# Optimization experiments

Measured on AMD Instinct MI355X. Metric: run time of the kernel, lower is better.

The kernel has to match this reference:

```python
import jax, jax.numpy as jnp
import numpy as np

D_MODEL, D_QKV, N_HEADS, D_FFN = 2048, 128, 16, 8192
B, L = 2, 2048
EPS = 1e-8
ROPE_THETA = 10000.0


def _rope_cos_sin(seq_len, dim, dtype):
    # interleaved RoPE (rotary_embedding_torch default): pairs (0,1),(2,3),...
    inv_freq = ROPE_THETA ** (-jnp.arange(0, dim, 2, dtype=jnp.float32) / dim)
    ang = jnp.arange(seq_len, dtype=jnp.float32)[:, None] * inv_freq[None, :]  # [L, dim/2]
    return jnp.cos(ang).astype(dtype), jnp.sin(ang).astype(dtype)


def _apply_rope(t, cos, sin):
    # t: [b, h, l, d]; cos/sin: [l, d/2]
    t1, t2 = t[..., 0::2], t[..., 1::2]
    r1 = t1 * cos - t2 * sin
    r2 = t1 * sin + t2 * cos
    return jnp.stack([r1, r2], axis=-1).reshape(t.shape)


def setup_inputs() -> dict:
    key = jax.random.key(0)
    ks = jax.random.split(key, 5)
    d_out = D_QKV * N_HEADS * 3 + D_FFN * 2  # 22528
    return {
        "x": jax.random.normal(ks[0], (B, L, D_MODEL), dtype=jnp.float32),
        "g": jnp.ones((D_MODEL,), dtype=jnp.float32),
        "W_dense": jax.random.normal(ks[1], (d_out, D_MODEL), dtype=jnp.float32) * 0.02,
        "b_dense": jnp.zeros((d_out,), dtype=jnp.float32),
        "W_attn_out": jax.random.normal(ks[2], (D_MODEL, D_QKV * N_HEADS), dtype=jnp.float32) * 0.02,
        "W_ffn_out": jax.random.normal(ks[3], (D_MODEL, D_FFN), dtype=jnp.float32) * 0.02,
    }


def reference(x, g, W_dense, b_dense, W_attn_out, W_ffn_out):
    # RMSNorm (torch.norm variant): x / clamp(||x|| * d^-0.5, eps) * g
    norm = jnp.sqrt(jnp.sum(x * x, axis=-1, keepdims=True)) * (D_MODEL ** -0.5)
    normed = x / jnp.maximum(norm, EPS) * g

    h = jnp.einsum('bld,od->blo', normed, W_dense) + b_dense  # [B, L, 22528]
    dh = D_QKV * N_HEADS
    q, k, v, a, b_gate = jnp.split(h, [dh, 2 * dh, 3 * dh, 3 * dh + D_FFN], axis=-1)

    def to_heads(t):
        return t.reshape(B, L, N_HEADS, D_QKV).transpose(0, 2, 1, 3)  # [b,h,l,d]

    q, k, v = to_heads(q), to_heads(k), to_heads(v)
    cos, sin = _rope_cos_sin(L, D_QKV, x.dtype)
    q = _apply_rope(q, cos, sin)
    k = _apply_rope(k, cos, sin)

    scale = 1.0 / jnp.sqrt(jnp.asarray(D_QKV, dtype=x.dtype))
    scores = jnp.einsum('bhqd,bhkd->bhqk', q, k) * scale
    causal = jnp.tril(jnp.ones((L, L), dtype=bool))
    scores = jnp.where(causal, scores, jnp.asarray(-jnp.inf, dtype=scores.dtype))
    probs = jax.nn.softmax(scores, axis=-1)
    attn = jnp.einsum('bhqk,bhkd->bqhd', probs, v).reshape(B, L, dh)

    attn_out = jnp.einsum('blk,ok->blo', attn, W_attn_out)
    ffn_out = jnp.einsum('blf,of->blo', a * jax.nn.silu(b_gate), W_ffn_out)
    return x + attn_out + ffn_out
```

## Files before the change

kernel.cpp:

```cpp
#include <hip/hip_runtime.h>
#include <hip/hip_bf16.h>
#include <cmath>

typedef __bf16 bf16;
typedef __attribute__((ext_vector_type(8))) __bf16 bf16x8;
typedef __attribute__((ext_vector_type(4))) float f32x4;
typedef unsigned int u32;
typedef unsigned short u16;

#define D_MODEL 2048
#define NH 16
#define DQ 128
#define DH 2048
#define DFFN 8192
#define DOUT 22528
#define BATCH 2
#define SEQ 2048
#define NROWS 4096

__device__ __forceinline__ void gload16(const void* g, void* l) {
    __builtin_amdgcn_global_load_lds((__attribute__((address_space(1))) const void*)g,
                                     (__attribute__((address_space(3))) void*)l, 16, 0, 0);
}

__device__ __forceinline__ float bf2f(u16 u) {
    union { u32 i; float f; } c; c.i = ((u32)u) << 16; return c.f;
}

__global__ __launch_bounds__(256) void cvt_f32_bf16(const float* __restrict__ in,
                                                    bf16* __restrict__ out) {
    size_t i = ((size_t)blockIdx.x * 256 + threadIdx.x) * 8;
    float4 a = *(const float4*)(in + i);
    float4 b = *(const float4*)(in + i + 4);
    bf16x8 o;
    o[0]=(bf16)a.x; o[1]=(bf16)a.y; o[2]=(bf16)a.z; o[3]=(bf16)a.w;
    o[4]=(bf16)b.x; o[5]=(bf16)b.y; o[6]=(bf16)b.z; o[7]=(bf16)b.w;
    *(bf16x8*)(out + i) = o;
}

__global__ __launch_bounds__(256) void rmsnorm_k(const float* __restrict__ x,
                                                 const float* __restrict__ g,
                                                 bf16* __restrict__ out) {
    __shared__ float red[4];
    const int row = blockIdx.x;
    const int t = threadIdx.x;
    const float* xr = x + (size_t)row * D_MODEL;
    float4 v0 = *(const float4*)(xr + t*8);
    float4 v1 = *(const float4*)(xr + t*8 + 4);
    float ss = v0.x*v0.x + v0.y*v0.y + v0.z*v0.z + v0.w*v0.w
             + v1.x*v1.x + v1.y*v1.y + v1.z*v1.z + v1.w*v1.w;
    #pragma unroll
    for (int m = 32; m >= 1; m >>= 1) ss += __shfl_xor(ss, m);
    if ((t & 63) == 0) red[t >> 6] = ss;
    __syncthreads();
    float tot = red[0] + red[1] + red[2] + red[3];
    float norm = sqrtf(tot) * 0.022097086912079608f;
    float inv = 1.0f / fmaxf(norm, 1e-8f);
    float4 g0 = *(const float4*)(g + t*8);
    float4 g1 = *(const float4*)(g + t*8 + 4);
    bf16x8 o;
    o[0]=(bf16)(v0.x*inv*g0.x); o[1]=(bf16)(v0.y*inv*g0.y);
    o[2]=(bf16)(v0.z*inv*g0.z); o[3]=(bf16)(v0.w*inv*g0.w);
    o[4]=(bf16)(v1.x*inv*g1.x); o[5]=(bf16)(v1.y*inv*g1.y);
    o[6]=(bf16)(v1.z*inv*g1.z); o[7]=(bf16)(v1.w*inv*g1.w);
    *(bf16x8*)(out + (size_t)row * D_MODEL + t*8) = o;
}

#define VMW(n)  asm volatile("s_waitcnt vmcnt(" #n ")" ::: "memory")
#define LGK0()  asm volatile("s_waitcnt lgkmcnt(0)" ::: "memory")
#define BARX()  { asm volatile("" ::: "memory"); __builtin_amdgcn_s_barrier(); asm volatile("" ::: "memory"); }

#define SLINE_A(c_, t_) \
    gload16(Asrc + (size_t)((c_)*64)*K + (size_t)(t_)*64, \
            smem + (((t_)&1)<<16) + (c_)*8192 + wid*1024);
#define SLINE_B(c_, t_) \
    gload16(Bsrc + (size_t)((c_)*64)*K + (size_t)(t_)*64, \
            smem + (((t_)&1)<<16) + 32768 + (c_)*8192 + wid*1024);

#define PH_READS_B() \
    _Pragma("unroll") for (int n = 0; n < 4; ++n) { \
        const char* p_ = bb + (wn*64 + n*16 + la) * 128; \
        bfr[n][0] = *(const bf16x8*)(p_ + pg0); \
        bfr[n][1] = *(const bf16x8*)(p_ + pg1); }

#define PH_READS_A(qd_) \
    _Pragma("unroll") for (int mm = 0; mm < 2; ++mm) { \
        const char* p_ = ab + (wm*128 + ((qd_)*2 + mm)*16 + la) * 128; \
        af[mm][0] = *(const bf16x8*)(p_ + pg0); \
        af[mm][1] = *(const bf16x8*)(p_ + pg1); }

#define PH_MFMA(qd_) \
    __builtin_amdgcn_s_setprio(1); \
    _Pragma("unroll") for (int mm = 0; mm < 2; ++mm) \
        _Pragma("unroll") for (int n = 0; n < 4; ++n) { \
            acc[(qd_)*2+mm][n] = __builtin_amdgcn_mfma_f32_16x16x32_bf16(af[mm][0], bfr[n][0], acc[(qd_)*2+mm][n], 0, 0, 0); \
            acc[(qd_)*2+mm][n] = __builtin_amdgcn_mfma_f32_16x16x32_bf16(af[mm][1], bfr[n][1], acc[(qd_)*2+mm][n], 0, 0, 0); } \
    __builtin_amdgcn_s_setprio(0);

template<int MODE>
__global__ __launch_bounds__(512, 2) void gemm256f(
    const bf16* __restrict__ A, const bf16* __restrict__ B,
    int M, int N, int K, int nbx,
    const float* __restrict__ bias, bf16* __restrict__ outb,
    const float* __restrict__ addsrc, float* __restrict__ outf)
{
    __shared__ char smem[131072];
    const int tid = threadIdx.x;
    const int wid = tid >> 6, lane = tid & 63;
    const int la = lane & 15, hi = lane >> 4;
    const int wm = wid >> 2, wn = wid & 3;

    const int nwg = gridDim.x;
    const int cpx = nwg >> 3;
    const int bI = blockIdx.x;
    const int wg = (bI & 7) * cpx + (bI >> 3);
    const int bm = wg / nbx, bn = wg % nbx;
    const size_t m0 = (size_t)bm * 256, n0 = (size_t)bn * 256;

    const int lr = lane >> 3, lg = lane & 7;
    const int sg = lg ^ lr;
    const bf16* Asrc = A + (m0 + wid*8 + lr) * (size_t)K + sg*8;
    const bf16* Bsrc = B + (n0 + wid*8 + lr) * (size_t)K + sg*8;

    const int pg0 = (hi ^ (la & 7)) << 4;
    const int pg1 = ((4 + hi) ^ (la & 7)) << 4;

    f32x4 acc[8][4] = {};
    const int NT = K >> 6;

    SLINE_A(0,0); SLINE_A(2,0);
    SLINE_B(0,0); SLINE_B(1,0);
    SLINE_B(2,0); SLINE_B(3,0);
    SLINE_A(1,0); SLINE_A(3,0);
    VMW(2);
    BARX();

    bf16x8 bfr[4][2];
    bf16x8 af[2][2];

    #pragma unroll 1
    for (int t = 0; t < NT - 1; ++t) {
        const char* ab = smem + ((t & 1) << 16);
        const char* bb = ab + 32768;
        const int nx = t + 1;
        PH_READS_B(); PH_READS_A(0);
        SLINE_A(0,nx); SLINE_A(2,nx);
        BARX(); LGK0(); PH_MFMA(0); BARX();
        PH_READS_A(1);
        SLINE_B(0,nx); SLINE_B(1,nx);
        BARX(); LGK0(); PH_MFMA(1); VMW(4); BARX();
        PH_READS_A(2);
        SLINE_B(2,nx); SLINE_B(3,nx);
        BARX(); LGK0(); PH_MFMA(2); BARX();
        PH_READS_A(3);
        SLINE_A(1,nx); SLINE_A(3,nx);
        BARX(); LGK0(); PH_MFMA(3); VMW(2); BARX();
    }
    {
        const int t = NT - 1;
        const char* ab = smem + ((t & 1) << 16);
        const char* bb = ab + 32768;
        PH_READS_B(); PH_READS_A(0);
        BARX(); LGK0(); PH_MFMA(0); BARX();
        PH_READS_A(1);
        BARX(); LGK0(); PH_MFMA(1); VMW(0); BARX();
        PH_READS_A(2);
        BARX(); LGK0(); PH_MFMA(2); BARX();
        PH_READS_A(3);
        BARX(); LGK0(); PH_MFMA(3); BARX();
    }

    #pragma unroll
    for (int mf = 0; mf < 8; ++mf) {
        const size_t row = m0 + wm*128 + mf*16 + hi*4;
        #pragma unroll
        for (int nf = 0; nf < 4; ++nf) {
            const size_t col = n0 + wn*64 + nf*16 + la;
            if (MODE == 0) {
                const float bv = bias[col];
                #pragma unroll
                for (int r = 0; r < 4; ++r)
                    outb[(row + r) * N + col] = (bf16)(acc[mf][nf][r] + bv);
            } else {
                #pragma unroll
                for (int r = 0; r < 4; ++r) {
                    const size_t off = (row + r) * N + col;
                    outf[off] = addsrc[off] + acc[mf][nf][r];
                }
            }
        }
    }
}

template<int MODE>
__global__ __launch_bounds__(256) void gemm_bt(
    const bf16* __restrict__ A, const bf16* __restrict__ B,
    int M, int N, int K,
    const float* __restrict__ bias, bf16* __restrict__ outb,
    const float* __restrict__ addsrc, float* __restrict__ outf)
{
    __shared__ bf16 As[128][32];
    __shared__ bf16 Bs[128][32];
    const int tid = threadIdx.x;
    const int wid = tid >> 6, lane = tid & 63;
    const int la = lane & 15, hi = lane >> 4;
    const int m0 = blockIdx.y * 128, n0 = blockIdx.x * 128;
    const int wr = (wid >> 1) * 64, wc = (wid & 1) * 64;
    f32x4 acc[4][4] = {};
    const int idx0 = tid, idx1 = 256 + tid;
    const int r0 = idx0 >> 2, c0 = (idx0 & 3) << 3;
    const int r1 = idx1 >> 2, c1 = (idx1 & 3) << 3;
    const bf16* Ap0 = A + (size_t)(m0 + r0) * K + c0;
    const bf16* Ap1 = A + (size_t)(m0 + r1) * K + c1;
    const bf16* Bp0 = B + (size_t)(n0 + r0) * K + c0;
    const bf16* Bp1 = B + (size_t)(n0 + r1) * K + c1;
    char* asb = (char*)As + wid * 1024;
    char* bsb = (char*)Bs + wid * 1024;

    for (int k0 = 0; k0 < K; k0 += 32) {
        __syncthreads();
        gload16(Ap0 + k0, asb);
        gload16(Ap1 + k0, asb + 4096);
        gload16(Bp0 + k0, bsb);
        gload16(Bp1 + k0, bsb + 4096);
        __syncthreads();
        bf16x8 af[4], bfr[4];
        #pragma unroll
        for (int m = 0; m < 4; ++m) af[m] = *(const bf16x8*)&As[wr + m*16 + la][hi*8];
        #pragma unroll
        for (int n = 0; n < 4; ++n) bfr[n] = *(const bf16x8*)&Bs[wc + n*16 + la][hi*8];
        #pragma unroll
        for (int m = 0; m < 4; ++m)
            #pragma unroll
            for (int n = 0; n < 4; ++n)
                acc[m][n] = __builtin_amdgcn_mfma_f32_16x16x32_bf16(af[m], bfr[n], acc[m][n], 0, 0, 0);
    }

    #pragma unroll
    for (int m = 0; m < 4; ++m) {
        const int row = m0 + wr + m*16 + hi*4;
        #pragma unroll
        for (int n = 0; n < 4; ++n) {
            const int col = n0 + wc + n*16 + la;
            if (MODE == 0) {
                const float bv = bias[col];
                #pragma unroll
                for (int r = 0; r < 4; ++r)
                    outb[(size_t)(row + r) * N + col] = (bf16)(acc[m][n][r] + bv);
            } else {
                #pragma unroll
                for (int r = 0; r < 4; ++r) {
                    const size_t off = (size_t)(row + r) * N + col;
                    outf[off] = addsrc[off] + acc[m][n][r];
                }
            }
        }
    }
}

__global__ __launch_bounds__(256) void rope_table(float* __restrict__ ctab,
                                                  float* __restrict__ stab) {
    int idx = blockIdx.x * 256 + threadIdx.x;
    int l = idx >> 6, i = idx & 63;
    float inv = powf(10000.0f, -(float)i / 64.0f);
    float ang = (float)l * inv;
    float s, c;
    sincosf(ang, &s, &c);
    ctab[idx] = c; stab[idx] = s;
}

__device__ __forceinline__ u32 rope_pair(u32 u, float c, float s) {
    float t1 = bf2f((u16)(u & 0xffff));
    float t2 = bf2f((u16)(u >> 16));
    float r1 = t1 * c - t2 * s;
    float r2 = t1 * s + t2 * c;
    bf16 b1 = (bf16)r1, b2 = (bf16)r2;
    return (u32)__builtin_bit_cast(u16, b1) | ((u32)__builtin_bit_cast(u16, b2) << 16);
}

__global__ __launch_bounds__(256) void rope_qk(const bf16* __restrict__ h,
                                               const float* __restrict__ ctab,
                                               const float* __restrict__ stab,
                                               bf16* __restrict__ qb, bf16* __restrict__ kb) {
    int idx = blockIdx.x * 256 + threadIdx.x;
    int i  = idx & 63;
    int hh = (idx >> 6) & 15;
    int l  = (idx >> 10) & 2047;
    int b  = idx >> 21;
    size_t hrow = (size_t)(b * SEQ + l) * DOUT;
    float c = ctab[l*64 + i], s = stab[l*64 + i];
    u32 uq = *(const u32*)(h + hrow + hh*DQ + 2*i);
    u32 uk = *(const u32*)(h + hrow + DH + hh*DQ + 2*i);
    size_t orow = ((size_t)(b*NH + hh) * SEQ + l) * DQ + 2*i;
    *(u32*)(qb + orow) = rope_pair(uq, c, s);
    *(u32*)(kb + orow) = rope_pair(uk, c, s);
}

__global__ __launch_bounds__(256) void v_transpose(const bf16* __restrict__ h,
                                                   bf16* __restrict__ vt) {
    __shared__ u32 lds[64][68];
    const int lt = blockIdx.x, bh = blockIdx.y;
    const int b = bh >> 4, hh = bh & 15;
    const int t = threadIdx.x;
    const bf16* src = h + (size_t)(b * SEQ + lt * 64) * DOUT + 2*DH + hh * DQ;
    #pragma unroll
    for (int i = 0; i < 4; ++i) {
        int j = i*256 + t;
        int l = j >> 4, ch = j & 15;
        uint4 v = *(const uint4*)(src + (size_t)l * DOUT + ch*8);
        *(uint4*)&lds[l][ch*4] = v;
    }
    __syncthreads();
    bf16* dst = vt + (size_t)bh * DQ * SEQ + lt * 64;
    #pragma unroll
    for (int i = 0; i < 4; ++i) {
        int j = i*256 + t;
        int d = j >> 3, lc = j & 7;
        u32 out[4];
        #pragma unroll
        for (int m = 0; m < 4; ++m) {
            u32 a0 = lds[lc*8 + 2*m][d >> 1];
            u32 a1 = lds[lc*8 + 2*m + 1][d >> 1];
            u16 s0 = (d & 1) ? (u16)(a0 >> 16) : (u16)(a0 & 0xffff);
            u16 s1 = (d & 1) ? (u16)(a1 >> 16) : (u16)(a1 & 0xffff);
            out[m] = (u32)s0 | ((u32)s1 << 16);
        }
        *(uint4*)(dst + (size_t)d * SEQ + lc*8) = *(uint4*)out;
    }
}

__global__ __launch_bounds__(256) void silu_k(const bf16* __restrict__ h,
                                              bf16* __restrict__ ag) {
    size_t idx = ((size_t)blockIdx.x * 256 + threadIdx.x) * 8;
    int r = (int)(idx >> 13);
    int f = (int)(idx & 8191);
    const bf16* hr = h + (size_t)r * DOUT + 3*DH;
    bf16x8 va = *(const bf16x8*)(hr + f);
    bf16x8 vb = *(const bf16x8*)(hr + DFFN + f);
    bf16x8 o;
    #pragma unroll
    for (int j = 0; j < 8; ++j) {
        float a = (float)va[j];
        float b = (float)vb[j];
        float sil = b / (1.0f + __expf(-b));
        o[j] = (bf16)(a * sil);
    }
    *(bf16x8*)(ag + idx) = o;
}

__global__ __launch_bounds__(256) void attn_fa(const bf16* __restrict__ Q,
                                               const bf16* __restrict__ Kb,
                                               const bf16* __restrict__ Vt,
                                               bf16* __restrict__ O) {
    __shared__ bf16 Ks[64][128];
    __shared__ bf16 Vts[128][64];
    __shared__ bf16 Ps[4][16][64];
    const int qt = blockIdx.x, bh = blockIdx.y;
    const int b = bh >> 4, hh = bh & 15;
    const int tid = threadIdx.x, wid = tid >> 6, lane = tid & 63;
    const int la = lane & 15, hi = lane >> 4;
    const bf16* Qp = Q + (size_t)bh * SEQ * DQ;
    const bf16* Kp = Kb + (size_t)bh * SEQ * DQ;
    const bf16* Vp = Vt + (size_t)bh * DQ * SEQ;
    const int q0w = qt * 64 + wid * 16;

    bf16x8 qf[4];
    #pragma unroll
    for (int s = 0; s < 4; ++s)
        qf[s] = *(const bf16x8*)(Qp + (size_t)(q0w + la) * DQ + s*32 + hi*8);

    f32x4 acc_o[8] = {};
    float m_run[4] = {-1e30f, -1e30f, -1e30f, -1e30f};
    float l_run[4] = {0.f, 0.f, 0.f, 0.f};
    const float scale = 0.08838834764831845f;

    const int nk = qt + 1;
    for (int kt = 0; kt < nk; ++kt) {
        const int k0 = kt * 64;
        __syncthreads();
        #pragma unroll
        for (int i = 0; i < 4; ++i) {
            int j = i*256 + tid;
            int kr = j >> 4, jg = j & 15;
            gload16(Kp + (size_t)(k0 + kr) * DQ + ((jg ^ (kr & 7)) << 3),
                    (char*)Ks + i*4096 + wid*1024);
            int d = j >> 3, vg = j & 7;
            gload16(Vp + (size_t)d * SEQ + k0 + ((vg ^ (d & 7)) << 3),
                    (char*)Vts + i*4096 + wid*1024);
        }
        __syncthreads();

        f32x4 sacc[4] = {};
        __builtin_amdgcn_s_setprio(1);
        #pragma unroll
        for (int g = 0; g < 4; ++g) {
            const int krow = g*16 + la;
            #pragma unroll
            for (int s = 0; s < 4; ++s) {
                bf16x8 kf = *(const bf16x8*)((const char*)Ks + krow*256 + (((s*4 + hi) ^ (la & 7)) << 4));
                sacc[g] = __builtin_amdgcn_mfma_f32_16x16x32_bf16(qf[s], kf, sacc[g], 0, 0, 0);
            }
        }
        __builtin_amdgcn_s_setprio(0);

        float mnew[4];
        #pragma unroll
        for (int r = 0; r < 4; ++r) mnew[r] = m_run[r];
        #pragma unroll
        for (int g = 0; g < 4; ++g)
            #pragma unroll
            for (int r = 0; r < 4; ++r) {
                float sv = sacc[g][r] * scale;
                int qi = q0w + hi*4 + r;
                int ki = k0 + g*16 + la;
                sv = (ki <= qi) ? sv : -1e30f;
                sacc[g][r] = sv;
                mnew[r] = fmaxf(mnew[r], sv);
            }
        #pragma unroll
        for (int r = 0; r < 4; ++r) {
            float v = mnew[r];
            v = fmaxf(v, __shfl_xor(v, 1));
            v = fmaxf(v, __shfl_xor(v, 2));
            v = fmaxf(v, __shfl_xor(v, 4));
            v = fmaxf(v, __shfl_xor(v, 8));
            mnew[r] = v;
        }
        float resc[4], lsum[4];
        #pragma unroll
        for (int r = 0; r < 4; ++r) {
            resc[r] = __expf(m_run[r] - mnew[r]);
            m_run[r] = mnew[r];
            lsum[r] = 0.f;
        }
        #pragma unroll
        for (int g = 0; g < 4; ++g)
            #pragma unroll
            for (int r = 0; r < 4; ++r) {
                float p = __expf(sacc[g][r] - mnew[r]);
                sacc[g][r] = p;
                lsum[r] += p;
            }
        #pragma unroll
        for (int r = 0; r < 4; ++r) {
            float v = lsum[r];
            v += __shfl_xor(v, 1); v += __shfl_xor(v, 2);
            v += __shfl_xor(v, 4); v += __shfl_xor(v, 8);
            l_run[r] = l_run[r] * resc[r] + v;
        }
        #pragma unroll
        for (int g = 0; g < 4; ++g)
            #pragma unroll
            for (int r = 0; r < 4; ++r) {
                int prow = hi*4 + r;
                int pcol = (g*16 + la) ^ ((prow & 7) << 3);
                Ps[wid][prow][pcol] = (bf16)sacc[g][r];
            }
        #pragma unroll
        for (int n = 0; n < 8; ++n)
            #pragma unroll
            for (int r = 0; r < 4; ++r) acc_o[n][r] *= resc[r];
        __builtin_amdgcn_s_setprio(1);
        #pragma unroll
        for (int kk = 0; kk < 2; ++kk) {
            bf16x8 pf = *(const bf16x8*)((const char*)&Ps[wid][0][0] + la*128 +
                                         (((kk*32 + hi*8) ^ ((la & 7) << 3)) << 1));
            #pragma unroll
            for (int n = 0; n < 8; ++n) {
                const int vrow = n*16 + la;
                bf16x8 vf = *(const bf16x8*)((const char*)Vts + vrow*128 + (((kk*4 + hi) ^ (la & 7)) << 4));
                acc_o[n] = __builtin_amdgcn_mfma_f32_16x16x32_bf16(pf, vf, acc_o[n], 0, 0, 0);
            }
        }
        __builtin_amdgcn_s_setprio(0);
    }

    bf16* Op = O + (size_t)b * SEQ * DH + (size_t)hh * DQ;
    #pragma unroll
    for (int r = 0; r < 4; ++r) {
        int qi = q0w + hi*4 + r;
        float invl = 1.0f / l_run[r];
        #pragma unroll
        for (int n = 0; n < 8; ++n)
            Op[(size_t)qi * DH + n*16 + la] = (bf16)(acc_o[n][r] * invl);
    }
}

extern "C" void kernel_launch(void* const* d_in, const int* in_sizes, int n_in,
                              void* d_out, int out_size, void* d_ws, size_t ws_size,
                              hipStream_t stream) {
    const float* x       = (const float*)d_in[0];
    const float* g       = (const float*)d_in[1];
    const float* W_dense = (const float*)d_in[2];
    const float* b_dense = (const float*)d_in[3];
    const float* W_attn  = (const float*)d_in[4];
    const float* W_ffn   = (const float*)d_in[5];
    float* out = (float*)d_out;

    char* ws = (char*)d_ws;
    bf16* normed  = (bf16*)(ws + 0);
    bf16* Wd_b    = (bf16*)(ws + 16777216);
    bf16* Wa_b    = (bf16*)(ws + 109051904);
    bf16* Wf_b    = (bf16*)(ws + 117440512);
    bf16* h_b     = (bf16*)(ws + 150994944);
    bf16* ag_b    = (bf16*)(ws + 335544320);
    float* ctab   = (float*)(ws + 402653184);
    float* stab   = (float*)(ws + 403177472);
    bf16* q_b  = (bf16*)(ws + 16777216);
    bf16* k_b  = (bf16*)(ws + 16777216 + 16777216);
    bf16* vt_b = (bf16*)(ws + 16777216 + 33554432);
    bf16* attn_b = normed;

    cvt_f32_bf16<<<46137344/2048, 256, 0, stream>>>(W_dense, Wd_b);
    cvt_f32_bf16<<<4194304/2048, 256, 0, stream>>>(W_attn, Wa_b);
    cvt_f32_bf16<<<16777216/2048, 256, 0, stream>>>(W_ffn, Wf_b);
    rmsnorm_k<<<NROWS, 256, 0, stream>>>(x, g, normed);
    {
        dim3 grid((NROWS/256) * (DOUT/256));
        gemm256f<0><<<grid, 512, 0, stream>>>(normed, Wd_b, NROWS, DOUT, D_MODEL,
                                              DOUT/256, b_dense, h_b, nullptr, nullptr);
    }
    rope_table<<<SEQ*64/256, 256, 0, stream>>>(ctab, stab);
    rope_qk<<<4194304/256, 256, 0, stream>>>(h_b, ctab, stab, q_b, k_b);
    {
        dim3 grid(SEQ/64, BATCH*NH);
        v_transpose<<<grid, 256, 0, stream>>>(h_b, vt_b);
    }
    silu_k<<<(size_t)NROWS*DFFN/8/256, 256, 0, stream>>>(h_b, ag_b);
    {
        dim3 grid(SEQ/64, BATCH*NH);
        attn_fa<<<grid, 256, 0, stream>>>(q_b, k_b, vt_b, attn_b);
    }
    {
        dim3 grid(D_MODEL/128, NROWS/128);
        gemm_bt<1><<<grid, 256, 0, stream>>>(attn_b, Wa_b, NROWS, D_MODEL, DH,
                                             nullptr, nullptr, x, out);
    }
    {
        dim3 grid(D_MODEL/128, NROWS/128);
        gemm_bt<1><<<grid, 256, 0, stream>>>(ag_b, Wf_b, NROWS, D_MODEL, DFFN,
                                             nullptr, nullptr, out, out);
    }
}
```

Before: 952.8 us.

## Fuse attention and FFN output projections into one pipelined GEMM

```diff
diff --git a/kernel.cpp b/kernel.cpp
--- a/kernel.cpp
+++ b/kernel.cpp
@@ -26,6 +26,10 @@
 __device__ __forceinline__ float bf2f(u16 u) {
     union { u32 i; float f; } c; c.i = ((u32)u) << 16; return c.f;
 }
+
+#define VMW(n)  asm volatile("s_waitcnt vmcnt(" #n ")" ::: "memory")
+#define LGK0()  asm volatile("s_waitcnt lgkmcnt(0)" ::: "memory")
+#define BARX()  { asm volatile("" ::: "memory"); __builtin_amdgcn_s_barrier(); asm volatile("" ::: "memory"); }
 
 __global__ __launch_bounds__(256) void cvt_f32_bf16(const float* __restrict__ in,
                                                     bf16* __restrict__ out) {
@@ -65,10 +69,6 @@
     o[6]=(bf16)(v1.z*inv*g1.z); o[7]=(bf16)(v1.w*inv*g1.w);
     *(bf16x8*)(out + (size_t)row * D_MODEL + t*8) = o;
 }
-
-#define VMW(n)  asm volatile("s_waitcnt vmcnt(" #n ")" ::: "memory")
-#define LGK0()  asm volatile("s_waitcnt lgkmcnt(0)" ::: "memory")
-#define BARX()  { asm volatile("" ::: "memory"); __builtin_amdgcn_s_barrier(); asm volatile("" ::: "memory"); }
 
 #define SLINE_A(c_, t_) \
     gload16(Asrc + (size_t)((c_)*64)*K + (size_t)(t_)*64, \
@@ -192,67 +192,100 @@
     }
 }
 
-template<int MODE>
-__global__ __launch_bounds__(256) void gemm_bt(
-    const bf16* __restrict__ A, const bf16* __restrict__ B,
-    int M, int N, int K,
-    const float* __restrict__ bias, bf16* __restrict__ outb,
-    const float* __restrict__ addsrc, float* __restrict__ outf)
+#define OSTAGE_A(st_, c_) { \
+    const bf16* s_ = (st_) < 32 ? A1s + (size_t)((c_)*64)*2048 + (size_t)(st_)*64 \
+                                : A2s + (size_t)((c_)*64)*8192 + (size_t)((st_)-32)*64; \
+    gload16(s_, smem + ((st_)%3)*49152 + (c_)*8192 + wid*1024); }
+#define OSTAGE_B(st_, c_) { \
+    const bf16* s_ = (st_) < 32 ? B1s + (size_t)((c_)*64)*2048 + (size_t)(st_)*64 \
+                                : B2s + (size_t)((c_)*64)*8192 + (size_t)((st_)-32)*64; \
+    gload16(s_, smem + ((st_)%3)*49152 + 16384 + (c_)*8192 + wid*1024); }
+
+__global__ __launch_bounds__(512, 2) void gemm_out(
+    const bf16* __restrict__ A1, const bf16* __restrict__ B1,
+    const bf16* __restrict__ A2, const bf16* __restrict__ B2,
+    const float* __restrict__ x, float* __restrict__ outf)
 {
-    __shared__ bf16 As[128][32];
-    __shared__ bf16 Bs[128][32];
+    __shared__ char smem[147456];
     const int tid = threadIdx.x;
     const int wid = tid >> 6, lane = tid & 63;
     const int la = lane & 15, hi = lane >> 4;
-    const int m0 = blockIdx.y * 128, n0 = blockIdx.x * 128;
-    const int wr = (wid >> 1) * 64, wc = (wid & 1) * 64;
+    const int wm = wid >> 2, wn = wid & 3;
+
+    const int nwg = gridDim.x;
+    const int cpx = nwg >> 3;
+    const int bI = blockIdx.x;
+    const int wg = (bI & 7) * cpx + (bI >> 3);
+    const int bm = wg >> 3, bn = wg & 7;
+    const size_t m0 = (size_t)bm * 128, n0 = (size_t)bn * 256;
+
+    const int lr = lane >> 3, lg = lane & 7;
+    const int sg = lg ^ lr;
+    const bf16* A1s = A1 + (m0 + wid*8 + lr) * (size_t)2048 + sg*8;
+    const bf16* A2s = A2 + (m0 + wid*8 + lr) * (size_t)8192 + sg*8;
+    const bf16* B1s = B1 + (n0 + wid*8 + lr) * (size_t)2048 + sg*8;
+    const bf16* B2s = B2 + (n0 + wid*8 + lr) * (size_t)8192 + sg*8;
+
+    const int pg0 = (hi ^ (la & 7)) << 4;
+    const int pg1 = ((4 + hi) ^ (la & 7)) << 4;
+
     f32x4 acc[4][4] = {};
-    const int idx0 = tid, idx1 = 256 + tid;
-    const int r0 = idx0 >> 2, c0 = (idx0 & 3) << 3;
-    const int r1 = idx1 >> 2, c1 = (idx1 & 3) << 3;
-    const bf16* Ap0 = A + (size_t)(m0 + r0) * K + c0;
-    const bf16* Ap1 = A + (size_t)(m0 + r1) * K + c1;
-    const bf16* Bp0 = B + (size_t)(n0 + r0) * K + c0;
-    const bf16* Bp1 = B + (size_t)(n0 + r1) * K + c1;
-    char* asb = (char*)As + wid * 1024;
-    char* bsb = (char*)Bs + wid * 1024;
-
-    for (int k0 = 0; k0 < K; k0 += 32) {
-        __syncthreads();
-        gload16(Ap0 + k0, asb);
-        gload16(Ap1 + k0, asb + 4096);
-        gload16(Bp0 + k0, bsb);
-        gload16(Bp1 + k0, bsb + 4096);
-        __syncthreads();
-        bf16x8 af[4], bfr[4];
-        #pragma unroll
-        for (int m = 0; m < 4; ++m) af[m] = *(const bf16x8*)&As[wr + m*16 + la][hi*8];
-        #pragma unroll
-        for (int n = 0; n < 4; ++n) bfr[n] = *(const bf16x8*)&Bs[wc + n*16 + la][hi*8];
+    const int NT = 160;
+
+    OSTAGE_A(0,0); OSTAGE_A(0,1);
+    OSTAGE_B(0,0); OSTAGE_B(0,1); OSTAGE_B(0,2); OSTAGE_B(0,3);
+    OSTAGE_A(1,0); OSTAGE_A(1,1);
+    OSTAGE_B(1,0); OSTAGE_B(1,1); OSTAGE_B(1,2); OSTAGE_B(1,3);
+    VMW(6);
+    BARX();
+
+    bf16x8 af[4], bfr[4];
+    #pragma unroll 1
+    for (int t = 0; t < NT; ++t) {
+        const char* ab = smem + (t % 3) * 49152;
+        const char* bb = ab + 16384;
+        const int st = t + 2;
+        #pragma unroll
+        for (int m = 0; m < 4; ++m) af[m]  = *(const bf16x8*)(ab + (wm*64 + m*16 + la)*128 + pg0);
+        #pragma unroll
+        for (int n = 0; n < 4; ++n) bfr[n] = *(const bf16x8*)(bb + (wn*64 + n*16 + la)*128 + pg0);
+        if (st < NT) { OSTAGE_A(st,0); OSTAGE_A(st,1); OSTAGE_B(st,0); }
+        BARX(); LGK0();
+        __builtin_amdgcn_s_setprio(1);
         #pragma unroll
         for (int m = 0; m < 4; ++m)
             #pragma unroll
             for (int n = 0; n < 4; ++n)
                 acc[m][n] = __builtin_amdgcn_mfma_f32_16x16x32_bf16(af[m], bfr[n], acc[m][n], 0, 0, 0);
-    }
-
-    #pragma unroll
-    for (int m = 0; m < 4; ++m) {
-        const int row = m0 + wr + m*16 + hi*4;
-        #pragma unroll
-        for (int n = 0; n < 4; ++n) {
-            const int col = n0 + wc + n*16 + la;
-            if (MODE == 0) {
-                const float bv = bias[col];
-                #pragma unroll
-                for (int r = 0; r < 4; ++r)
-                    outb[(size_t)(row + r) * N + col] = (bf16)(acc[m][n][r] + bv);
-            } else {
-                #pragma unroll
-                for (int r = 0; r < 4; ++r) {
-                    const size_t off = (size_t)(row + r) * N + col;
-                    outf[off] = addsrc[off] + acc[m][n][r];
-                }
+        __builtin_amdgcn_s_setprio(0);
+        BARX();
+        #pragma unroll
+        for (int m = 0; m < 4; ++m) af[m]  = *(const bf16x8*)(ab + (wm*64 + m*16 + la)*128 + pg1);
+        #pragma unroll
+        for (int n = 0; n < 4; ++n) bfr[n] = *(const bf16x8*)(bb + (wn*64 + n*16 + la)*128 + pg1);
+        if (st < NT) { OSTAGE_B(st,1); OSTAGE_B(st,2); OSTAGE_B(st,3); }
+        if (t < NT - 2) { VMW(6); } else { VMW(0); }
+        BARX(); LGK0();
+        __builtin_amdgcn_s_setprio(1);
+        #pragma unroll
+        for (int m = 0; m < 4; ++m)
+            #pragma unroll
+            for (int n = 0; n < 4; ++n)
+                acc[m][n] = __builtin_amdgcn_mfma_f32_16x16x32_bf16(af[m], bfr[n], acc[m][n], 0, 0, 0);
+        __builtin_amdgcn_s_setprio(0);
+        BARX();
+    }
+
+    #pragma unroll
+    for (int mf = 0; mf < 4; ++mf) {
+        const size_t row = m0 + wm*64 + mf*16 + hi*4;
+        #pragma unroll
+        for (int nf = 0; nf < 4; ++nf) {
+            const size_t col = n0 + wn*64 + nf*16 + la;
+            #pragma unroll
+            for (int r = 0; r < 4; ++r) {
+                const size_t off = (row + r) * (size_t)DH + col;
+                outf[off] = x[off] + acc[mf][nf][r];
             }
         }
     }
@@ -531,14 +564,5 @@
         dim3 grid(SEQ/64, BATCH*NH);
         attn_fa<<<grid, 256, 0, stream>>>(q_b, k_b, vt_b, attn_b);
     }
-    {
-        dim3 grid(D_MODEL/128, NROWS/128);
-        gemm_bt<1><<<grid, 256, 0, stream>>>(attn_b, Wa_b, NROWS, D_MODEL, DH,
-                                             nullptr, nullptr, x, out);
-    }
-    {
-        dim3 grid(D_MODEL/128, NROWS/128);
-        gemm_bt<1><<<grid, 256, 0, stream>>>(ag_b, Wf_b, NROWS, D_MODEL, DFFN,
-                                             nullptr, nullptr, out, out);
-    }
-}
+    gemm_out<<<256, 512, 0, stream>>>(attn_b, Wa_b, ag_b, Wf_b, x, out);
+}
```

After: 845.9 us. -11.2%, faster.
